# Kernel optimization log

Hardware: AMD Instinct MI355X
Metric: run time of the kernel (lower is better)

The kernel has to match this reference:

```python
import jax, jax.numpy as jnp
import numpy as np

C = 256
SHAPE = (4, 256, 32, 32, 32)  # B, C, D, H, W


def setup_inputs() -> dict:
    key = jax.random.key(0)
    ks = jax.random.split(key, 8)
    scale = 1.0 / np.sqrt(C)
    return {
        "x": jax.random.normal(ks[0], SHAPE, dtype=jnp.float32),
        "y": jax.random.normal(ks[1], SHAPE, dtype=jnp.float32),
        "Wq": jax.random.normal(ks[2], (C, C), dtype=jnp.float32) * scale,
        "bq": jax.random.normal(ks[3], (C,), dtype=jnp.float32) * 0.01,
        "Wk": jax.random.normal(ks[4], (C, C), dtype=jnp.float32) * scale,
        "bk": jax.random.normal(ks[5], (C,), dtype=jnp.float32) * 0.01,
        "Wv": jax.random.normal(ks[6], (C, C), dtype=jnp.float32) * scale,
        "bv": jax.random.normal(ks[7], (C,), dtype=jnp.float32) * 0.01,
    }


def _proj_flat(v, W, b):
    # 1x1x1 Conv3d == per-voxel linear over channels. v: [B,C,D,H,W] -> [B,C,N]
    B, Cc = v.shape[0], v.shape[1]
    vf = v.reshape(B, Cc, -1)  # [B, C, N]
    return jnp.einsum("oc,bcn->bon", W, vf) + b[None, :, None]


def reference(x, y, Wq, bq, Wk, bk, Wv, bv):
    spatial = y.shape[2:]
    q = _proj_flat(x, Wq, bq)  # [B, C, N]
    k = _proj_flat(y, Wk, bk)  # [B, C, N]
    v = _proj_flat(y, Wv, bv)  # [B, C, N]
    # channel-attention: scores[b, i, j] = sum_n q[b,i,n] * k[b,j,n]  (unscaled)
    scores = jnp.einsum("bin,bjn->bij", q, k)  # [B, C, C]
    weights = jax.nn.softmax(scores, axis=2)
    fused = jnp.einsum("bij,bjn->bin", weights, v)  # [B, C, N]
    return fused.reshape(fused.shape[0], fused.shape[1], *spatial)
```

## Files before the change

kernel.cpp:

```cpp
#include <hip/hip_runtime.h>

#define Bb 4
#define Cc 256
#define Nn 32768

typedef short s16x8 __attribute__((ext_vector_type(8)));
typedef float f32x4 __attribute__((ext_vector_type(4)));

__device__ __forceinline__ unsigned short bfh(float f) {
    union { float f; unsigned u; } c; c.f = f;
    unsigned u = c.u + 0x7fffu + ((c.u >> 16) & 1u);
    return (unsigned short)(u >> 16);
}
__device__ __forceinline__ unsigned fbits(float f) {
    union { float f; unsigned u; } c; c.f = f; return c.u;
}
__device__ __forceinline__ float fof(unsigned u) {
    union { unsigned u; float f; } c; c.u = u; return c.f;
}
__device__ __forceinline__ int swz(int l) { return l ^ ((l >> 3) & 6); }

__device__ __forceinline__ void cvt8(float4 A, float4 B, uint4& h, uint4& l) {
    unsigned a0 = fbits(A.x), a1 = fbits(A.y), a2 = fbits(A.z), a3 = fbits(A.w);
    unsigned b0 = fbits(B.x), b1 = fbits(B.y), b2 = fbits(B.z), b3 = fbits(B.w);
    h.x = __builtin_amdgcn_perm(a1, a0, 0x07060302u);
    h.y = __builtin_amdgcn_perm(a3, a2, 0x07060302u);
    h.z = __builtin_amdgcn_perm(b1, b0, 0x07060302u);
    h.w = __builtin_amdgcn_perm(b3, b2, 0x07060302u);
    unsigned l0 = fbits(A.x - fof(a0 & 0xffff0000u)) + 0x8000u;
    unsigned l1 = fbits(A.y - fof(a1 & 0xffff0000u)) + 0x8000u;
    unsigned l2 = fbits(A.z - fof(a2 & 0xffff0000u)) + 0x8000u;
    unsigned l3 = fbits(A.w - fof(a3 & 0xffff0000u)) + 0x8000u;
    unsigned m0 = fbits(B.x - fof(b0 & 0xffff0000u)) + 0x8000u;
    unsigned m1 = fbits(B.y - fof(b1 & 0xffff0000u)) + 0x8000u;
    unsigned m2 = fbits(B.z - fof(b2 & 0xffff0000u)) + 0x8000u;
    unsigned m3 = fbits(B.w - fof(b3 & 0xffff0000u)) + 0x8000u;
    l.x = __builtin_amdgcn_perm(l1, l0, 0x07060302u);
    l.y = __builtin_amdgcn_perm(l3, l2, 0x07060302u);
    l.z = __builtin_amdgcn_perm(m1, m0, 0x07060302u);
    l.w = __builtin_amdgcn_perm(m3, m2, 0x07060302u);
}
__device__ __forceinline__ float s4(float4 v) { return (v.x + v.y) + (v.z + v.w); }

__global__ __launch_bounds__(512, 2) void k_gram(const float* __restrict__ x,
                                                 const float* __restrict__ y,
                                                 float* __restrict__ part,
                                                 float* __restrict__ sxp,
                                                 float* __restrict__ syp,
                                                 int nsplit) {
    int G = Bb * nsplit * 2;
    int chunk = G >> 3;
    int lid = blockIdx.x;
    int bid = (lid & 7) * chunk + (lid >> 3);

    int half = bid & 1;
    int ks = (bid >> 1) % nsplit;
    int b = bid / (2 * nsplit);
    int Kblk = Nn / nsplit;
    int nstep = Kblk >> 5;

    const float* X = x + (size_t)b * Cc * Nn + (size_t)(half * 128) * Nn + (size_t)ks * Kblk;
    const float* Y = y + (size_t)b * Cc * Nn + (size_t)ks * Kblk;

    __shared__ __align__(16) short XH[4096], XL[4096];
    __shared__ __align__(16) short YH[8192], YL[8192];

    int tid = threadIdx.x;
    int lane = tid & 63;
    int wave = tid >> 6;
    int wr = wave >> 2, wc = wave & 3;

    int xr = tid >> 2, xq = tid & 3;
    const float* px = X + (size_t)xr * Nn + xq * 8;
    int xl = (xr & 15) + 16 * xq;
    int xo = ((xr >> 4) * 64 + swz(xl)) * 8;
    int yr = tid >> 1, yh2 = tid & 1;
    const float* py = Y + (size_t)yr * Nn + yh2 * 16;
    int yl0 = (yr & 15) + 32 * yh2, yl1 = yl0 + 16;
    int yo0 = ((yr >> 4) * 64 + swz(yl0)) * 8;
    int yo1 = ((yr >> 4) * 64 + swz(yl1)) * 8;

    f32x4 acc[4][4];
    #pragma unroll
    for (int i = 0; i < 4; ++i)
        #pragma unroll
        for (int j = 0; j < 4; ++j)
            #pragma unroll
            for (int z = 0; z < 4; ++z) acc[i][j][z] = 0.f;

    float xsum = 0.f, ysum = 0.f;
    float4 A0[2], B0[4], A1[2], B1[4];

    #define LDX(A, B, kb) do { \
        A[0] = ((const float4*)(px + (kb)))[0]; A[1] = ((const float4*)(px + (kb)))[1]; \
        B[0] = ((const float4*)(py + (kb)))[0]; B[1] = ((const float4*)(py + (kb)))[1]; \
        B[2] = ((const float4*)(py + (kb)))[2]; B[3] = ((const float4*)(py + (kb)))[3]; \
    } while (0)

    #define COMPUTE do { \
        int sl = swz(lane); \
        s16x8 ah[4], al[4]; \
        _Pragma("unroll") \
        for (int i = 0; i < 4; ++i) { \
            int fr = (wr * 4 + i) * 64 + sl; \
            ah[i] = *(const s16x8*)&XH[fr * 8]; \
            al[i] = *(const s16x8*)&XL[fr * 8]; \
        } \
        _Pragma("unroll") \
        for (int j = 0; j < 4; ++j) { \
            int fr = (wc * 4 + j) * 64 + sl; \
            s16x8 bh = *(const s16x8*)&YH[fr * 8]; \
            s16x8 bl = *(const s16x8*)&YL[fr * 8]; \
            _Pragma("unroll") \
            for (int i = 0; i < 4; ++i) { \
                acc[i][j] = __builtin_amdgcn_mfma_f32_16x16x32_bf16(ah[i], bh, acc[i][j], 0, 0, 0); \
                acc[i][j] = __builtin_amdgcn_mfma_f32_16x16x32_bf16(ah[i], bl, acc[i][j], 0, 0, 0); \
                acc[i][j] = __builtin_amdgcn_mfma_f32_16x16x32_bf16(al[i], bh, acc[i][j], 0, 0, 0); \
            } \
        } \
    } while (0)

    #define GSTEP(A, B, nkb, donext) do { \
        uint4 hx, qxv, hy0, qy0, hy1, qy1; \
        cvt8(A[0], A[1], hx, qxv); \
        cvt8(B[0], B[1], hy0, qy0); \
        cvt8(B[2], B[3], hy1, qy1); \
        xsum += s4(A[0]) + s4(A[1]); \
        if (half == 0) ysum += s4(B[0]) + s4(B[1]) + s4(B[2]) + s4(B[3]); \
        __syncthreads(); \
        *(uint4*)&XH[xo] = hx;  *(uint4*)&XL[xo] = qxv; \
        *(uint4*)&YH[yo0] = hy0; *(uint4*)&YL[yo0] = qy0; \
        *(uint4*)&YH[yo1] = hy1; *(uint4*)&YL[yo1] = qy1; \
        if (donext) LDX(A, B, nkb); \
        __syncthreads(); \
        COMPUTE; \
    } while (0)

    LDX(A0, B0, 0);
    LDX(A1, B1, 32);
    for (int t = 0; t < nstep; t += 2) {
        GSTEP(A0, B0, (t + 2) * 32, t + 2 < nstep);
        GSTEP(A1, B1, (t + 3) * 32, t + 3 < nstep);
    }
    #undef GSTEP
    #undef COMPUTE
    #undef LDX

    xsum += __shfl_xor(xsum, 1);
    xsum += __shfl_xor(xsum, 2);
    ysum += __shfl_xor(ysum, 1);
    if (xq == 0) sxp[((size_t)b * nsplit + ks) * 256 + half * 128 + xr] = xsum;
    if (half == 0 && yh2 == 0) syp[((size_t)b * nsplit + ks) * 256 + yr] = ysum;

    float* P = part + ((size_t)b * nsplit + ks) * Cc * Cc;
    #pragma unroll
    for (int i = 0; i < 4; ++i)
        #pragma unroll
        for (int j = 0; j < 4; ++j)
            #pragma unroll
            for (int reg = 0; reg < 4; ++reg) {
                int gi = half * 128 + wr * 64 + i * 16 + (lane >> 4) * 4 + reg;
                int gj = wc * 64 + j * 16 + (lane & 15);
                P[(size_t)gi * Cc + gj] = acc[i][j][reg];
            }
}

__global__ __launch_bounds__(256) void k_reduceS(const float* __restrict__ part,
                                                 const float* __restrict__ sxp,
                                                 const float* __restrict__ syp,
                                                 float* __restrict__ S,
                                                 float* __restrict__ sx,
                                                 float* __restrict__ sy, int split) {
    if (blockIdx.x < 256) {
        int t = blockIdx.x * 256 + threadIdx.x;
        int b = t >> 14;
        int rc = t & 16383;
        float4 s = {0.f, 0.f, 0.f, 0.f};
        for (int ks = 0; ks < split; ++ks) {
            float4 v = ((const float4*)(part + (((size_t)b * split + ks) << 16)))[rc];
            s.x += v.x; s.y += v.y; s.z += v.z; s.w += v.w;
        }
        ((float4*)S)[t] = s;
    } else {
        int flat = (blockIdx.x - 256) * 256 + threadIdx.x;
        int b = flat >> 9, rem = flat & 511, which = rem >> 8, c = rem & 255;
        const float* src = (which ? syp : sxp) + (size_t)b * split * 256 + c;
        float s = 0.f;
        for (int ks = 0; ks < split; ++ks) s += src[(size_t)ks * 256];
        (which ? sy : sx)[b * 256 + c] = s;
    }
}

__global__ __launch_bounds__(256) void k_attn(const float* __restrict__ S,
                                              const float* __restrict__ sx,
                                              const float* __restrict__ sy,
                                              const float* __restrict__ Wq,
                                              const float* __restrict__ Wk,
                                              const float* __restrict__ Wv,
                                              const float* __restrict__ bq,
                                              const float* __restrict__ bk,
                                              const float* __restrict__ bv,
                                              short* __restrict__ Mbf,
                                              float* __restrict__ cb) {
    __shared__ float wq_lds[8][256];
    __shared__ float u_lds[8][256];
    __shared__ float p_lds[8][256];
    __shared__ float wv_lds[32][256];
    __shared__ float sx_lds[256], sy_lds[256];
    __shared__ float qx_lds[8];

    int b = blockIdx.x >> 5;
    int i0 = (blockIdx.x & 31) << 3;
    int tid = threadIdx.x;
    int lane = tid & 63, wv4 = tid >> 6;

    float bqv[8];
    #pragma unroll
    for (int ii = 0; ii < 8; ++ii) {
        wq_lds[ii][tid] = Wq[(size_t)(i0 + ii) * Cc + tid];
        bqv[ii] = bq[i0 + ii];
    }
    sx_lds[tid] = sx[b * Cc + tid];
    sy_lds[tid] = sy[b * Cc + tid];
    __syncthreads();

    float u[8] = {};
    const float* Sb = S + (size_t)b * Cc * Cc + tid;
    #pragma unroll 4
    for (int c = 0; c < Cc; ++c) {
        float s = Sb[(size_t)c * Cc];
        #pragma unroll
        for (int ii = 0; ii < 8; ++ii) u[ii] += wq_lds[ii][c] * s;
    }
    #pragma unroll
    for (int ii = 0; ii < 8; ++ii) u_lds[ii][tid] = u[ii] + bqv[ii] * sy_lds[tid];

    #pragma unroll
    for (int rr = 0; rr < 2; ++rr) {
        int ii = wv4 * 2 + rr;
        float p = 0.f;
        #pragma unroll
        for (int k = 0; k < 4; ++k) { int c = lane + 64 * k; p += wq_lds[ii][c] * sx_lds[c]; }
        #pragma unroll
        for (int m = 1; m < 64; m <<= 1) p += __shfl_xor(p, m);
        if (lane == 0) qx_lds[ii] = p;
    }
    __syncthreads();

    float sc[8] = {};
    const float* WkRow = Wk + (size_t)tid * Cc;
    for (int ch = 0; ch < 8; ++ch) {
        float wkr[32];
        #pragma unroll
        for (int k = 0; k < 8; ++k)
            *(float4*)&wkr[4 * k] = ((const float4*)(WkRow + ch * 32))[k];
        #pragma unroll
        for (int dd = 0; dd < 32; ++dd) {
            float w = wkr[dd];
            #pragma unroll
            for (int ii = 0; ii < 8; ++ii) sc[ii] += u_lds[ii][ch * 32 + dd] * w;
        }
    }
    float bkj = bk[tid];
    #pragma unroll
    for (int ii = 0; ii < 8; ++ii) {
        sc[ii] += (qx_lds[ii] + 32768.0f * bqv[ii]) * bkj;
        p_lds[ii][tid] = sc[ii];
    }
    __syncthreads();

    #pragma unroll
    for (int rr = 0; rr < 2; ++rr) {
        int ii = wv4 * 2 + rr;
        float v0 = p_lds[ii][lane], v1 = p_lds[ii][lane + 64];
        float v2 = p_lds[ii][lane + 128], v3 = p_lds[ii][lane + 192];
        float mx = fmaxf(fmaxf(v0, v1), fmaxf(v2, v3));
        #pragma unroll
        for (int m = 1; m < 64; m <<= 1) mx = fmaxf(mx, __shfl_xor(mx, m));
        float e0 = expf(v0 - mx), e1 = expf(v1 - mx), e2 = expf(v2 - mx), e3 = expf(v3 - mx);
        float ssum = (e0 + e1) + (e2 + e3);
        #pragma unroll
        for (int m = 1; m < 64; m <<= 1) ssum += __shfl_xor(ssum, m);
        float inv = 1.0f / ssum;
        float w0 = e0 * inv, w1 = e1 * inv, w2 = e2 * inv, w3 = e3 * inv;
        p_lds[ii][lane] = w0; p_lds[ii][lane + 64] = w1;
        p_lds[ii][lane + 128] = w2; p_lds[ii][lane + 192] = w3;
        float cbp = w0 * bv[lane] + w1 * bv[lane + 64] + w2 * bv[lane + 128] + w3 * bv[lane + 192];
        #pragma unroll
        for (int m = 1; m < 64; m <<= 1) cbp += __shfl_xor(cbp, m);
        if (lane == 0) cb[b * Cc + i0 + ii] = cbp;
    }
    __syncthreads();

    float m[8] = {};
    for (int jc = 0; jc < 8; ++jc) {
        #pragma unroll
        for (int k = 0; k < 8; ++k) {
            int fidx = k * 256 + tid;
            int jj = fidx >> 6, f4 = fidx & 63;
            *(float4*)&wv_lds[jj][4 * f4] =
                *(const float4*)(Wv + (size_t)(jc * 32 + jj) * Cc + 4 * f4);
        }
        __syncthreads();
        #pragma unroll 4
        for (int jj = 0; jj < 32; ++jj) {
            float w = wv_lds[jj][tid];
            #pragma unroll
            for (int ii = 0; ii < 8; ++ii) m[ii] += p_lds[ii][jc * 32 + jj] * w;
        }
        __syncthreads();
    }
    #pragma unroll
    for (int ii = 0; ii < 8; ++ii)
        Mbf[((size_t)(b * Cc + i0 + ii)) * Cc + tid] = (short)bfh(m[ii]);
}

__global__ __launch_bounds__(512, 2) void k_out_mfma(const short* __restrict__ Mbf,
                                                     const float* __restrict__ y,
                                                     const float* __restrict__ cb,
                                                     float* __restrict__ out) {
    int tid = threadIdx.x;
    int lane = tid & 63;
    int wave = tid >> 6;
    int wr = wave >> 2, wc = wave & 3;
    int bid = blockIdx.x;
    int b = bid >> 8, grp = bid & 255;
    int nbase = grp * 128 + wc * 32;
    const float* Y = y + (size_t)b * Cc * Nn;
    const short* M = Mbf + (size_t)b * Cc * Cc;
    int l15 = lane & 15;
    int cbase = 8 * (lane >> 4);
    int n0 = nbase + l15;

    f32x4 acc[8][2];
    #pragma unroll
    for (int ti = 0; ti < 8; ++ti)
        #pragma unroll
        for (int nb = 0; nb < 2; ++nb)
            #pragma unroll
            for (int z = 0; z < 4; ++z) acc[ti][nb][z] = 0.f;

    s16x8 af0[8], af1[8];
    float ya0[8], yb0[8], ya1[8], yb1[8];

    #define AFLD(AF, s) do { int c0 = 32 * (s) + cbase; \
        _Pragma("unroll") \
        for (int ti = 0; ti < 8; ++ti) \
            AF[ti] = *(const s16x8*)&M[(size_t)(wr * 128 + ti * 16 + l15) * Cc + c0]; \
        } while (0)

    #define LDY(YA, YB, s) do { int c0 = 32 * (s) + cbase; \
        _Pragma("unroll") \
        for (int j = 0; j < 8; ++j) { \
            YA[j] = Y[(size_t)(c0 + j) * Nn + n0]; \
            YB[j] = Y[(size_t)(c0 + j) * Nn + n0 + 16]; \
        } } while (0)

    #define OSTEP(AF, AFN, YA, YB, s) do { \
        s16x8 bf0, bf1; \
        _Pragma("unroll") \
        for (int j = 0; j < 8; ++j) { bf0[j] = (short)bfh(YA[j]); bf1[j] = (short)bfh(YB[j]); } \
        if ((s) + 1 < 8) AFLD(AFN, (s) + 1); \
        if ((s) + 2 < 8) LDY(YA, YB, (s) + 2); \
        _Pragma("unroll") \
        for (int ti = 0; ti < 8; ++ti) { \
            acc[ti][0] = __builtin_amdgcn_mfma_f32_16x16x32_bf16(AF[ti], bf0, acc[ti][0], 0, 0, 0); \
            acc[ti][1] = __builtin_amdgcn_mfma_f32_16x16x32_bf16(AF[ti], bf1, acc[ti][1], 0, 0, 0); \
        } } while (0)

    AFLD(af0, 0);
    LDY(ya0, yb0, 0);
    LDY(ya1, yb1, 1);
    for (int s = 0; s < 8; s += 2) {
        OSTEP(af0, af1, ya0, yb0, s);
        OSTEP(af1, af0, ya1, yb1, s + 1);
    }
    #undef OSTEP
    #undef LDY
    #undef AFLD

    #pragma unroll
    for (int ti = 0; ti < 8; ++ti)
        #pragma unroll
        for (int nb = 0; nb < 2; ++nb)
            #pragma unroll
            for (int reg = 0; reg < 4; ++reg) {
                int i = wr * 128 + ti * 16 + (lane >> 4) * 4 + reg;
                out[((size_t)b * Cc + i) * Nn + nbase + nb * 16 + l15] =
                    acc[ti][nb][reg] + cb[b * Cc + i];
            }
}

extern "C" void kernel_launch(void* const* d_in, const int* in_sizes, int n_in,
                              void* d_out, int out_size, void* d_ws, size_t ws_size,
                              hipStream_t stream) {
    const float* x  = (const float*)d_in[0];
    const float* y  = (const float*)d_in[1];
    const float* Wq = (const float*)d_in[2];
    const float* bq = (const float*)d_in[3];
    const float* Wk = (const float*)d_in[4];
    const float* bk = (const float*)d_in[5];
    const float* Wv = (const float*)d_in[6];
    const float* bv = (const float*)d_in[7];
    float* out = (float*)d_out;

    float* ws = (float*)d_ws;
    size_t off = 0;
    float* S  = ws + off; off += (size_t)Bb * Cc * Cc;
    float* sx = ws + off; off += Bb * Cc;
    float* sy = ws + off; off += Bb * Cc;
    short* Mbf = (short*)(ws + off); off += (size_t)Bb * Cc * Cc / 2;
    float* cb = ws + off; off += Bb * Cc;
    float* sxp = ws + off; off += (size_t)Bb * 64 * 256;
    float* syp = ws + off; off += (size_t)Bb * 64 * 256;
    float* part = ws + off;

    size_t avail = ws_size / 4 - off;
    int split = 32;
    while (split > 16 && (size_t)split * Bb * Cc * Cc > avail) split >>= 1;

    k_gram<<<Bb * split * 2, 512, 0, stream>>>(x, y, part, sxp, syp, split);
    k_reduceS<<<264, 256, 0, stream>>>(part, sxp, syp, S, sx, sy, split);
    k_attn<<<Bb * 32, 256, 0, stream>>>(S, sx, sy, Wq, Wk, Wv, bq, bk, bv, Mbf, cb);
    k_out_mfma<<<1024, 512, 0, stream>>>(Mbf, y, cb, out);
}
```

Baseline: 232.8 us.

## Split gram kernel X rows into quarters to double block count

The gram kernel now splits the 256 X channels into four 64-row quarters instead of two 128-row halves, which doubles the grid to Bb*split*4 blocks and halves the per-block accumulator tile. The goal is more blocks to fill the GPU and less register pressure per thread. The cost is that every Y tile (all 256 rows) is loaded and converted twice as often. That raises global traffic on y and the conversion work relative to MFMA work, and only half the threads load X.

Result: slower. 260.9 us (+12.1%).

```diff
diff --git a/kernel.cpp b/kernel.cpp
--- a/kernel.cpp
+++ b/kernel.cpp
@@ -48,21 +48,21 @@
                                                  float* __restrict__ sxp,
                                                  float* __restrict__ syp,
                                                  int nsplit) {
-    int G = Bb * nsplit * 2;
+    int G = Bb * nsplit * 4;
     int chunk = G >> 3;
     int lid = blockIdx.x;
     int bid = (lid & 7) * chunk + (lid >> 3);
 
-    int half = bid & 1;
-    int ks = (bid >> 1) % nsplit;
-    int b = bid / (2 * nsplit);
+    int q  = bid & 3;
+    int ks = (bid >> 2) % nsplit;
+    int b  = bid / (4 * nsplit);
     int Kblk = Nn / nsplit;
     int nstep = Kblk >> 5;
 
-    const float* X = x + (size_t)b * Cc * Nn + (size_t)(half * 128) * Nn + (size_t)ks * Kblk;
+    const float* X = x + (size_t)b * Cc * Nn + (size_t)(q * 64) * Nn + (size_t)ks * Kblk;
     const float* Y = y + (size_t)b * Cc * Nn + (size_t)ks * Kblk;
 
-    __shared__ __align__(16) short XH[4096], XL[4096];
+    __shared__ __align__(16) short XH[2048], XL[2048];
     __shared__ __align__(16) short YH[8192], YL[8192];
 
     int tid = threadIdx.x;
@@ -70,39 +70,41 @@
     int wave = tid >> 6;
     int wr = wave >> 2, wc = wave & 3;
 
-    int xr = tid >> 2, xq = tid & 3;
-    const float* px = X + (size_t)xr * Nn + xq * 8;
-    int xl = (xr & 15) + 16 * xq;
-    int xo = ((xr >> 4) * 64 + swz(xl)) * 8;
-    int yr = tid >> 1, yh2 = tid & 1;
-    const float* py = Y + (size_t)yr * Nn + yh2 * 16;
-    int yl0 = (yr & 15) + 32 * yh2, yl1 = yl0 + 16;
-    int yo0 = ((yr >> 4) * 64 + swz(yl0)) * 8;
-    int yo1 = ((yr >> 4) * 64 + swz(yl1)) * 8;
-
-    f32x4 acc[4][4];
-    #pragma unroll
-    for (int i = 0; i < 4; ++i)
+    bool isx = tid < 256;
+    int sxr = tid >> 2, sxh = tid & 3;
+    const float* px = X + (size_t)sxr * Nn + sxh * 8;
+    int xo = ((sxr >> 4) * 64 + swz((sxr & 15) + 16 * sxh)) * 8;
+
+    int yrA = tid >> 2, yhA = tid & 3;
+    const float* pyA = Y + (size_t)yrA * Nn + yhA * 8;
+    int yoA = ((yrA >> 4) * 64 + swz((yrA & 15) + 16 * yhA)) * 8;
+    int yrB = 128 + (tid >> 2);
+    const float* pyB = Y + (size_t)yrB * Nn + yhA * 8;
+    int yoB = ((yrB >> 4) * 64 + swz((yrB & 15) + 16 * yhA)) * 8;
+
+    f32x4 acc[2][4];
+    #pragma unroll
+    for (int i = 0; i < 2; ++i)
         #pragma unroll
         for (int j = 0; j < 4; ++j)
             #pragma unroll
             for (int z = 0; z < 4; ++z) acc[i][j][z] = 0.f;
 
-    float xsum = 0.f, ysum = 0.f;
-    float4 A0[2], B0[4], A1[2], B1[4];
+    float xsum = 0.f, ysA = 0.f, ysB = 0.f;
+    float4 A0[2], A1[2], B0[4], B1[4];
 
     #define LDX(A, B, kb) do { \
-        A[0] = ((const float4*)(px + (kb)))[0]; A[1] = ((const float4*)(px + (kb)))[1]; \
-        B[0] = ((const float4*)(py + (kb)))[0]; B[1] = ((const float4*)(py + (kb)))[1]; \
-        B[2] = ((const float4*)(py + (kb)))[2]; B[3] = ((const float4*)(py + (kb)))[3]; \
+        if (isx) { A[0] = ((const float4*)(px + (kb)))[0]; A[1] = ((const float4*)(px + (kb)))[1]; } \
+        B[0] = ((const float4*)(pyA + (kb)))[0]; B[1] = ((const float4*)(pyA + (kb)))[1]; \
+        B[2] = ((const float4*)(pyB + (kb)))[0]; B[3] = ((const float4*)(pyB + (kb)))[1]; \
     } while (0)
 
     #define COMPUTE do { \
         int sl = swz(lane); \
-        s16x8 ah[4], al[4]; \
-        _Pragma("unroll") \
-        for (int i = 0; i < 4; ++i) { \
-            int fr = (wr * 4 + i) * 64 + sl; \
+        s16x8 ah[2], al[2]; \
+        _Pragma("unroll") \
+        for (int i = 0; i < 2; ++i) { \
+            int fr = (wr * 2 + i) * 64 + sl; \
             ah[i] = *(const s16x8*)&XH[fr * 8]; \
             al[i] = *(const s16x8*)&XL[fr * 8]; \
         } \
@@ -112,7 +114,7 @@
             s16x8 bh = *(const s16x8*)&YH[fr * 8]; \
             s16x8 bl = *(const s16x8*)&YL[fr * 8]; \
             _Pragma("unroll") \
-            for (int i = 0; i < 4; ++i) { \
+            for (int i = 0; i < 2; ++i) { \
                 acc[i][j] = __builtin_amdgcn_mfma_f32_16x16x32_bf16(ah[i], bh, acc[i][j], 0, 0, 0); \
                 acc[i][j] = __builtin_amdgcn_mfma_f32_16x16x32_bf16(ah[i], bl, acc[i][j], 0, 0, 0); \
                 acc[i][j] = __builtin_amdgcn_mfma_f32_16x16x32_bf16(al[i], bh, acc[i][j], 0, 0, 0); \
@@ -121,16 +123,15 @@
     } while (0)
 
     #define GSTEP(A, B, nkb, donext) do { \
-        uint4 hx, qxv, hy0, qy0, hy1, qy1; \
-        cvt8(A[0], A[1], hx, qxv); \
-        cvt8(B[0], B[1], hy0, qy0); \
-        cvt8(B[2], B[3], hy1, qy1); \
-        xsum += s4(A[0]) + s4(A[1]); \
-        if (half == 0) ysum += s4(B[0]) + s4(B[1]) + s4(B[2]) + s4(B[3]); \
+        uint4 hx, qx2, hyA, qyA, hyB, qyB; \
+        if (isx) { cvt8(A[0], A[1], hx, qx2); xsum += s4(A[0]) + s4(A[1]); } \
+        cvt8(B[0], B[1], hyA, qyA); \
+        cvt8(B[2], B[3], hyB, qyB); \
+        if (q == 0) { ysA += s4(B[0]) + s4(B[1]); ysB += s4(B[2]) + s4(B[3]); } \
         __syncthreads(); \
-        *(uint4*)&XH[xo] = hx;  *(uint4*)&XL[xo] = qxv; \
-        *(uint4*)&YH[yo0] = hy0; *(uint4*)&YL[yo0] = qy0; \
-        *(uint4*)&YH[yo1] = hy1; *(uint4*)&YL[yo1] = qy1; \
+        if (isx) { *(uint4*)&XH[xo] = hx; *(uint4*)&XL[xo] = qx2; } \
+        *(uint4*)&YH[yoA] = hyA; *(uint4*)&YL[yoA] = qyA; \
+        *(uint4*)&YH[yoB] = hyB; *(uint4*)&YL[yoB] = qyB; \
         if (donext) LDX(A, B, nkb); \
         __syncthreads(); \
         COMPUTE; \
@@ -148,18 +149,23 @@
 
     xsum += __shfl_xor(xsum, 1);
     xsum += __shfl_xor(xsum, 2);
-    ysum += __shfl_xor(ysum, 1);
-    if (xq == 0) sxp[((size_t)b * nsplit + ks) * 256 + half * 128 + xr] = xsum;
-    if (half == 0 && yh2 == 0) syp[((size_t)b * nsplit + ks) * 256 + yr] = ysum;
+    ysA += __shfl_xor(ysA, 1); ysA += __shfl_xor(ysA, 2);
+    ysB += __shfl_xor(ysB, 1); ysB += __shfl_xor(ysB, 2);
+    size_t sbase = ((size_t)b * nsplit + ks) * 256;
+    if (isx && (tid & 3) == 0) sxp[sbase + q * 64 + sxr] = xsum;
+    if (q == 0 && (tid & 3) == 0) {
+        syp[sbase + yrA] = ysA;
+        syp[sbase + yrB] = ysB;
+    }
 
     float* P = part + ((size_t)b * nsplit + ks) * Cc * Cc;
     #pragma unroll
-    for (int i = 0; i < 4; ++i)
+    for (int i = 0; i < 2; ++i)
         #pragma unroll
         for (int j = 0; j < 4; ++j)
             #pragma unroll
             for (int reg = 0; reg < 4; ++reg) {
-                int gi = half * 128 + wr * 64 + i * 16 + (lane >> 4) * 4 + reg;
+                int gi = q * 64 + wr * 32 + i * 16 + (lane >> 4) * 4 + reg;
                 int gj = wc * 64 + j * 16 + (lane & 15);
                 P[(size_t)gi * Cc + gj] = acc[i][j][reg];
             }
@@ -419,7 +425,7 @@
     int split = 32;
     while (split > 16 && (size_t)split * Bb * Cc * Cc > avail) split >>= 1;
 
-    k_gram<<<Bb * split * 2, 512, 0, stream>>>(x, y, part, sxp, syp, split);
+    k_gram<<<Bb * split * 4, 512, 0, stream>>>(x, y, part, sxp, syp, split);
     k_reduceS<<<264, 256, 0, stream>>>(part, sxp, syp, S, sx, sy, split);
     k_attn<<<Bb * 32, 256, 0, stream>>>(S, sx, sy, Wq, Wk, Wv, bq, bk, bv, Mbf, cb);
     k_out_mfma<<<1024, 512, 0, stream>>>(Mbf, y, cb, out);
```
